# Kernel optimization log

Hardware: AMD Instinct MI355X
Metric: run time of the kernel (lower is better)

## Reference

```python
import jax, jax.numpy as jnp
import numpy as np

T = 500_000  # sequence length
K = 16       # number of hidden states


def setup_inputs() -> dict:
    key = jax.random.key(0)
    k1, k2, k3, k4 = jax.random.split(key, 4)
    y = jax.random.normal(k1, (T,), dtype=jnp.float32)
    transition_logits = jax.random.normal(k2, (K, K), dtype=jnp.float32)
    mu = 2.0 * jax.random.normal(k3, (K,), dtype=jnp.float32)
    log_sigma = 0.1 * jax.random.normal(k4, (K,), dtype=jnp.float32)
    return {"y": y, "transition_logits": transition_logits, "mu": mu, "log_sigma": log_sigma}


def _stationary_distribution(P):
    # Solve pi P = pi, sum(pi) = 1 via least squares (normal equations: differentiable, jit-safe).
    k = P.shape[0]
    A = jnp.concatenate([P.T - jnp.eye(k, dtype=P.dtype), jnp.ones((1, k), dtype=P.dtype)], axis=0)
    b = jnp.concatenate([jnp.zeros((k,), dtype=P.dtype), jnp.ones((1,), dtype=P.dtype)])
    return jnp.linalg.solve(A.T @ A, A.T @ b)


def reference(y, transition_logits, mu, log_sigma):
    P = jax.nn.softmax(transition_logits, axis=-1)  # [K, K] row-stochastic transition matrix
    sigma = jnp.exp(log_sigma)
    # Gaussian emission densities g[t, k] = N(y_t; mu_k, sigma_k^2)
    z = (y[:, None] - mu[None, :]) / sigma[None, :]
    INV_SQRT_2PI = 0.3989422804014327
    g = jnp.exp(-0.5 * z * z) * (INV_SQRT_2PI / sigma)[None, :]  # [T, K]

    ut0 = _stationary_distribution(P)              # [K]
    g0 = g[0]
    ft0 = jnp.sum(ut0 * g0)                        # scalar
    utt0 = ut0 * g0 / ft0                          # [K]

    def step(utt_prev, gt):
        ut = utt_prev @ P                          # predictive dist [K]
        ft = jnp.sum(ut * gt)                      # normalizer
        utt = ut * gt / ft                         # filtered posterior [K]
        return utt, (ut, ft, utt)

    _, (Ut, ft_rest, Utt) = jax.lax.scan(step, utt0, g[1:])

    ut = jnp.concatenate([ut0[None, :], Ut], axis=0)       # [T, K]
    u_norm = jnp.concatenate([utt0[None, :], Utt], axis=0)  # [T, K]
    ft = jnp.concatenate([ft0[None], ft_rest], axis=0)      # [T]
    return (ut, u_norm, ft)
```

## Files before the change

### kernel.cpp

```cpp
#include <hip/hip_runtime.h>

#define CHUNK_L 32
#define WARMUP_W 16
#define PI_ITERS 48

typedef float v2f __attribute__((ext_vector_type(2)));

template<int K> __device__ __forceinline__ float bcast16(float v) {
    return __int_as_float(__builtin_amdgcn_update_dpp(
        0, __float_as_int(v), 0x150 | K, 0xF, 0xF, true));
}
template<int N> __device__ __forceinline__ float rowror16(float v) {
    return __int_as_float(__builtin_amdgcn_update_dpp(
        0, __float_as_int(v), 0x120 | N, 0xF, 0xF, true));
}
__device__ __forceinline__ float rowsum16(float p) {
    p += rowror16<1>(p);
    p += rowror16<2>(p);
    p += rowror16<4>(p);
    p += rowror16<8>(p);
    return p;
}
__device__ __forceinline__ float rowmax16(float p) {
    p = fmaxf(p, rowror16<1>(p));
    p = fmaxf(p, rowror16<2>(p));
    p = fmaxf(p, rowror16<4>(p));
    p = fmaxf(p, rowror16<8>(p));
    return p;
}

__device__ __forceinline__ float dot16(float a, const v2f* pc2) {
    v2f b0, b1, u01, u23;
    b0.x = bcast16<0>(a);  b0.y = bcast16<1>(a);
    b1.x = bcast16<2>(a);  b1.y = bcast16<3>(a);
    u01 = b0 * pc2[0];
    u23 = b1 * pc2[1];
    b0.x = bcast16<4>(a);  b0.y = bcast16<5>(a);
    b1.x = bcast16<6>(a);  b1.y = bcast16<7>(a);
    u01 = b0 * pc2[2] + u01;
    u23 = b1 * pc2[3] + u23;
    b0.x = bcast16<8>(a);  b0.y = bcast16<9>(a);
    b1.x = bcast16<10>(a); b1.y = bcast16<11>(a);
    u01 = b0 * pc2[4] + u01;
    u23 = b1 * pc2[5] + u23;
    b0.x = bcast16<12>(a); b0.y = bcast16<13>(a);
    b1.x = bcast16<14>(a); b1.y = bcast16<15>(a);
    u01 = b0 * pc2[6] + u01;
    u23 = b1 * pc2[7] + u23;
    v2f u = u01 + u23;
    return u.x + u.y;
}

__global__ __launch_bounds__(256, 4) void hmm_filter_kernel(
    const float* __restrict__ y,
    const float* __restrict__ logits,
    const float* __restrict__ mu,
    const float* __restrict__ log_sigma,
    float* __restrict__ out,
    int T, int nchunks)
{
    __shared__ float Plds[256];

    const int tid = (int)threadIdx.x;
    const int j   = tid & 15;
    const int g   = tid >> 4;

    const float l  = logits[tid];
    const float mx = rowmax16(l);
    const float e  = __builtin_amdgcn_exp2f((l - mx) * 1.4426950408889634f);
    const float Pv = e * __builtin_amdgcn_rcpf(rowsum16(e));
    Plds[tid] = Pv;
    __syncthreads();

    v2f pc2[8];
    #pragma unroll
    for (int k = 0; k < 8; ++k) {
        pc2[k].x = Plds[(2 * k)     * 16 + j];
        pc2[k].y = Plds[(2 * k + 1) * 16 + j];
    }

    const int chunk = (int)blockIdx.x * 16 + g;
    if (chunk >= nchunks) return;

    float api = 0.0625f;
    #pragma unroll
    for (int i = 0; i < PI_ITERS; ++i) api = dot16(api, pc2);
    api *= __builtin_amdgcn_rcpf(rowsum16(api));

    const float isj = __expf(-log_sigma[j]);
    const float nmj = -mu[j] * isj;
    const float lcf = __log2f(0.3989422804014327f * isj);
    const float K2  = -0.7213475204444817f;
    auto emis = [&](float yt) -> float {
        float z = fmaf(yt, isj, nmj);
        return __builtin_amdgcn_exp2f(fmaf(z * z, K2, lcf));
    };

    const int wfrom = chunk * CHUNK_L;
    int t0 = wfrom - WARMUP_W; if (t0 < 0) t0 = 0;
    const bool first = (wfrom == 0);

    const float4* yb = (const float4*)(y + t0);
    float4 Y[12];
    #pragma unroll
    for (int i = 0; i < 12; ++i) Y[i] = yb[i];

    float p = api;
    #pragma unroll
    for (int i = 0; i < 4; ++i) {
        const float4 c4 = Y[i];
        p = dot16(p, pc2) * emis(c4.x);
        p = dot16(p, pc2) * emis(c4.y);
        p = dot16(p, pc2) * emis(c4.z);
        p = dot16(p, pc2) * emis(c4.w);
        if (i == 1) p *= __builtin_amdgcn_rcpf(rowsum16(p));
    }
    p *= __builtin_amdgcn_rcpf(rowsum16(p));
    if (first) p = api;

    float4 M[8];
    #pragma unroll
    for (int i = 0; i < 8; ++i) M[i] = first ? Y[i] : Y[i + 4];

    float* __restrict__ pU = out + (wfrom << 4) + j;
    float* __restrict__ pN = pU + (T << 4);
    float* __restrict__ pF = out + (T << 5) + wfrom;

    #pragma unroll
    for (int b = 0; b < 8; ++b) {
        const float4 c4 = M[b];
        const float g0 = emis(c4.x), g1 = emis(c4.y);
        const float g2 = emis(c4.z), g3 = emis(c4.w);

        const float q0  = dot16(p, pc2);
        const float pg0 = q0 * g0;
        const float s0  = rowsum16(pg0);
        const float r0  = __builtin_amdgcn_rcpf(s0);
        const float q1  = dot16(pg0, pc2);
        const float pg1 = q1 * g1;
        const float s1  = rowsum16(pg1);
        const float r1  = __builtin_amdgcn_rcpf(s1);
        const float q2  = dot16(pg1, pc2);
        const float pg2 = q2 * g2;
        const float s2  = rowsum16(pg2);
        const float r2  = __builtin_amdgcn_rcpf(s2);
        const float q3  = dot16(pg2, pc2);
        const float pg3 = q3 * g3;
        const float s3  = rowsum16(pg3);
        const float r3  = __builtin_amdgcn_rcpf(s3);

        const int o = b * 64;
        pU[o]      = q0;
        pU[o + 16] = q1 * r0;
        pU[o + 32] = q2 * r1;
        pU[o + 48] = q3 * r2;
        pN[o]      = pg0 * r0;
        pN[o + 16] = pg1 * r1;
        pN[o + 32] = pg2 * r2;
        const float utt3 = pg3 * r3;
        pN[o + 48] = utt3;
        if (j == 0)
            *(float4*)(pF + b * 4) = make_float4(s0, s1 * r0, s2 * r1, s3 * r2);

        p = utt3;
    }
}

extern "C" void kernel_launch(void* const* d_in, const int* in_sizes, int n_in,
                              void* d_out, int out_size, void* d_ws, size_t ws_size,
                              hipStream_t stream) {
    const float* y      = (const float*)d_in[0];
    const float* logits = (const float*)d_in[1];
    const float* mu     = (const float*)d_in[2];
    const float* ls     = (const float*)d_in[3];
    float* out = (float*)d_out;
    const int T = in_sizes[0];

    const int nchunks = (T + CHUNK_L - 1) / CHUNK_L;
    const int blocks  = (nchunks + 15) / 16;
    hmm_filter_kernel<<<blocks, 256, 0, stream>>>(y, logits, mu, ls, out,
                                                  T, nchunks);
}
```

Before: 98.07 us.

## Split setup into separate kernel, halve chunk length, stream y loads

Moves the softmax of the transition matrix and the stationary-distribution power iteration into a one-block setup kernel that writes P and pi to workspace. The filter kernel now reads them from there instead of recomputing them in every block. The chunk length drops from 32 to 16, which doubles the parallel chunks, and y is loaded through a rolling prefetch instead of a large register array. Occupancy hint raised to 8. The trade-off is that the 16-step warmup per chunk now equals the output work, roughly doubling redundant recurrence compute, and the extra kernel launch adds overhead.

```diff
diff --git a/kernel.cpp b/kernel.cpp
--- a/kernel.cpp
+++ b/kernel.cpp
@@ -1,6 +1,6 @@
 #include <hip/hip_runtime.h>
 
-#define CHUNK_L 32
+#define CHUNK_L 16
 #define WARMUP_W 16
 #define PI_ITERS 48
 
@@ -51,16 +51,10 @@
     return u.x + u.y;
 }
 
-__global__ __launch_bounds__(256, 4) void hmm_filter_kernel(
-    const float* __restrict__ y,
-    const float* __restrict__ logits,
-    const float* __restrict__ mu,
-    const float* __restrict__ log_sigma,
-    float* __restrict__ out,
-    int T, int nchunks)
+__global__ __launch_bounds__(256) void hmm_setup_kernel(
+    const float* __restrict__ logits, float* __restrict__ ws)
 {
     __shared__ float Plds[256];
-
     const int tid = (int)threadIdx.x;
     const int j   = tid & 15;
     const int g   = tid >> 4;
@@ -69,6 +63,7 @@
     const float mx = rowmax16(l);
     const float e  = __builtin_amdgcn_exp2f((l - mx) * 1.4426950408889634f);
     const float Pv = e * __builtin_amdgcn_rcpf(rowsum16(e));
+    ws[j * 16 + g] = Pv;
     Plds[tid] = Pv;
     __syncthreads();
 
@@ -78,14 +73,38 @@
         pc2[k].x = Plds[(2 * k)     * 16 + j];
         pc2[k].y = Plds[(2 * k + 1) * 16 + j];
     }
-
-    const int chunk = (int)blockIdx.x * 16 + g;
-    if (chunk >= nchunks) return;
-
     float api = 0.0625f;
     #pragma unroll
     for (int i = 0; i < PI_ITERS; ++i) api = dot16(api, pc2);
     api *= __builtin_amdgcn_rcpf(rowsum16(api));
+    if (g == 0) ws[256 + j] = api;
+}
+
+__global__ __launch_bounds__(256, 8) void hmm_filter_kernel(
+    const float* __restrict__ y,
+    const float* __restrict__ mu,
+    const float* __restrict__ log_sigma,
+    const float* __restrict__ ws,
+    float* __restrict__ out,
+    int T, int nchunks)
+{
+    const int tid = (int)threadIdx.x;
+    const int j   = tid & 15;
+    const int g   = tid >> 4;
+
+    const int chunk = (int)blockIdx.x * 16 + g;
+    if (chunk >= nchunks) return;
+
+    v2f pc2[8];
+    const float4* colp = (const float4*)(ws + j * 16);
+    {
+        const float4 A = colp[0], B = colp[1], C = colp[2], D = colp[3];
+        pc2[0].x = A.x; pc2[0].y = A.y;  pc2[1].x = A.z; pc2[1].y = A.w;
+        pc2[2].x = B.x; pc2[2].y = B.y;  pc2[3].x = B.z; pc2[3].y = B.w;
+        pc2[4].x = C.x; pc2[4].y = C.y;  pc2[5].x = C.z; pc2[5].y = C.w;
+        pc2[6].x = D.x; pc2[6].y = D.y;  pc2[7].x = D.z; pc2[7].y = D.w;
+    }
+    const float api = ws[256 + j];
 
     const float isj = __expf(-log_sigma[j]);
     const float nmj = -mu[j] * isj;
@@ -98,37 +117,37 @@
 
     const int wfrom = chunk * CHUNK_L;
     int t0 = wfrom - WARMUP_W; if (t0 < 0) t0 = 0;
-    const bool first = (wfrom == 0);
-
-    const float4* yb = (const float4*)(y + t0);
-    float4 Y[12];
-    #pragma unroll
-    for (int i = 0; i < 12; ++i) Y[i] = yb[i];
+    const int Tm4 = T - 4;
+
+    int t = t0;
+    float4 c4 = *(const float4*)(y + t);
+    float4 n1 = *(const float4*)(y + t + 4);
 
     float p = api;
-    #pragma unroll
-    for (int i = 0; i < 4; ++i) {
-        const float4 c4 = Y[i];
-        p = dot16(p, pc2) * emis(c4.x);
-        p = dot16(p, pc2) * emis(c4.y);
-        p = dot16(p, pc2) * emis(c4.z);
-        p = dot16(p, pc2) * emis(c4.w);
-        if (i == 1) p *= __builtin_amdgcn_rcpf(rowsum16(p));
+
+    if (t0 < wfrom) {
+        #pragma unroll
+        for (int b = 0; b < 4; ++b) {
+            const float4 n2 = *(const float4*)(y + t + 8);
+            p = dot16(p, pc2) * emis(c4.x);
+            p = dot16(p, pc2) * emis(c4.y);
+            p = dot16(p, pc2) * emis(c4.z);
+            p = dot16(p, pc2) * emis(c4.w);
+            if (b == 1) p *= __builtin_amdgcn_rcpf(rowsum16(p));
+            c4 = n1; n1 = n2; t += 4;
+        }
     }
     p *= __builtin_amdgcn_rcpf(rowsum16(p));
-    if (first) p = api;
-
-    float4 M[8];
-    #pragma unroll
-    for (int i = 0; i < 8; ++i) M[i] = first ? Y[i] : Y[i + 4];
 
     float* __restrict__ pU = out + (wfrom << 4) + j;
     float* __restrict__ pN = pU + (T << 4);
     float* __restrict__ pF = out + (T << 5) + wfrom;
 
     #pragma unroll
-    for (int b = 0; b < 8; ++b) {
-        const float4 c4 = M[b];
+    for (int b = 0; b < 4; ++b) {
+        int p2 = t + 8; if (p2 > Tm4) p2 = Tm4;
+        const float4 n2 = *(const float4*)(y + p2);
+
         const float g0 = emis(c4.x), g1 = emis(c4.y);
         const float g2 = emis(c4.z), g3 = emis(c4.w);
 
@@ -163,6 +182,7 @@
             *(float4*)(pF + b * 4) = make_float4(s0, s1 * r0, s2 * r1, s3 * r2);
 
         p = utt3;
+        c4 = n1; n1 = n2; t += 4;
     }
 }
 
@@ -174,10 +194,13 @@
     const float* mu     = (const float*)d_in[2];
     const float* ls     = (const float*)d_in[3];
     float* out = (float*)d_out;
+    float* ws  = (float*)d_ws;
     const int T = in_sizes[0];
+
+    hmm_setup_kernel<<<1, 256, 0, stream>>>(logits, ws);
 
     const int nchunks = (T + CHUNK_L - 1) / CHUNK_L;
     const int blocks  = (nchunks + 15) / 16;
-    hmm_filter_kernel<<<blocks, 256, 0, stream>>>(y, logits, mu, ls, out,
+    hmm_filter_kernel<<<blocks, 256, 0, stream>>>(y, mu, ls, ws, out,
                                                   T, nchunks);
 }
```

New measurement: 96.32 us. No clear change (-1.8%).
